# Kernel optimization log

Hardware: AMD Instinct MI355X
Metric: run time of the kernel (lower is better)

## Reference

```python
import jax, jax.numpy as jnp
import numpy as np

B, F, S = 64, 1024, 256
H = 1024  # hidden_size == input_size (required by default forward path)


def setup_inputs() -> dict:
    key = jax.random.key(0)
    k1, k2, k3, k4 = jax.random.split(key, 4)
    stdv = 1.0 / (H ** 0.5)
    x = jax.random.normal(k1, (B, F, S), dtype=jnp.float32)
    W = jax.random.uniform(k2, (F, 4 * H), dtype=jnp.float32, minval=-stdv, maxval=stdv)
    U = jax.random.uniform(k3, (H, 4 * H), dtype=jnp.float32, minval=-stdv, maxval=stdv)
    bias = jax.random.uniform(k4, (4 * H,), dtype=jnp.float32, minval=-stdv, maxval=stdv)
    return {"x": x, "W": W, "U": U, "bias": bias}


def reference(x, W, U, bias):
    # x: [B, F, S]. Faithful to MotionLSTM.forward with init_states=None,
    # isSampling=False, output_frame=0:  c_t = f_t * x_t + i_t * g_t.
    batch, _, seq = x.shape
    HS = U.shape[0]
    # Precompute input projection once: [S, B, 4H]
    xW = jnp.einsum('bfs,fg->sbg', x, W)
    x_seq = jnp.transpose(x, (2, 0, 1))  # [S, B, F]
    h0 = jnp.zeros((batch, HS), dtype=x.dtype)
    c0 = jnp.zeros((batch, HS), dtype=x.dtype)

    def step(carry, inputs):
        h, c = carry
        xw_t, x_t = inputs
        gates = xw_t + h @ U + bias  # [B, 4H]
        i_t = jax.nn.sigmoid(gates[:, :HS])
        f_t = jax.nn.sigmoid(gates[:, HS:2 * HS])
        g_t = jnp.tanh(gates[:, 2 * HS:3 * HS])
        o_t = jax.nn.sigmoid(gates[:, 3 * HS:])
        c_new = f_t * x_t + i_t * g_t  # isSampling=False path
        h_new = o_t * jnp.tanh(c_new)
        return (h_new, c_new), h_new

    (h_T, c_T), hs = jax.lax.scan(step, (h0, c0), (xW, x_seq))
    hidden_seq = jnp.transpose(hs, (1, 2, 0))  # [B, H, S]
    return hidden_seq, h_T, c_T
```

## Files before the change

### kernel.cpp

```cpp
#include <hip/hip_runtime.h>
#include <hip/hip_bf16.h>

typedef float f32x4 __attribute__((ext_vector_type(4)));
typedef short short8 __attribute__((ext_vector_type(8)));
typedef __bf16 bf16x8 __attribute__((ext_vector_type(8)));

#define DI __device__ __forceinline__

constexpr int Bsz = 64;
constexpr int Fd  = 1024;
constexpr int Seq = 256;
constexpr int G4  = 4096;
constexpr int Mrows = Seq * Bsz;

DI float bf2f(unsigned short u) {
  union { unsigned int i; float f; } v; v.i = ((unsigned int)u) << 16; return v.f;
}
DI unsigned short f2bf(float f) {
  union { float ff; unsigned int i; } v; v.ff = f;
  unsigned int x = v.i;
  return (unsigned short)((x + 0x7fffu + ((x >> 16) & 1u)) >> 16);
}
DI float sigm(float x) { return 1.f / (1.f + __expf(-x)); }
DI float tanhfast(float x) {
  float e = __expf(-2.f * fabsf(x));
  float t = (1.f - e) / (1.f + e);
  return x < 0.f ? -t : t;
}
DI f32x4 mfma16(short8 a, short8 b, f32x4 c) {
  return __builtin_amdgcn_mfma_f32_16x16x32_bf16(
      __builtin_bit_cast(bf16x8, a), __builtin_bit_cast(bf16x8, b), c, 0, 0, 0);
}

__global__ void k_tx(const float* __restrict__ x, unsigned short* __restrict__ xs) {
  __shared__ float t[32][33];
  int b = blockIdx.z, f0 = blockIdx.y * 32, s0 = blockIdx.x * 32;
  int tx = threadIdx.x & 31, ty = threadIdx.x >> 5;
  const float* src = x + ((size_t)b * Fd + f0) * Seq + s0;
#pragma unroll
  for (int i = 0; i < 32; i += 8)
    t[ty + i][tx] = src[(size_t)(ty + i) * Seq + tx];
  __syncthreads();
#pragma unroll
  for (int i = 0; i < 32; i += 8) {
    int s = s0 + ty + i, f = f0 + tx;
    xs[((size_t)s * Bsz + b) * Fd + f] = f2bf(t[tx][ty + i]);
  }
}

__global__ void k_tw(const float* __restrict__ in, unsigned short* __restrict__ out) {
  __shared__ float t[32][33];
  int n0 = blockIdx.x * 32, k0 = blockIdx.y * 32;
  int tx = threadIdx.x & 31, ty = threadIdx.x >> 5;
#pragma unroll
  for (int i = 0; i < 32; i += 8)
    t[ty + i][tx] = in[(size_t)(k0 + ty + i) * G4 + n0 + tx];
  __syncthreads();
#pragma unroll
  for (int i = 0; i < 32; i += 8)
    out[(size_t)(n0 + ty + i) * 1024 + k0 + tx] = f2bf(t[tx][ty + i]);
}

__global__ void k_zero(unsigned int* p, int n) {
  int i = blockIdx.x * 256 + threadIdx.x;
  if (i < n) p[i] = 0u;
}

__launch_bounds__(256, 2)
__global__ void k_gemm(const unsigned short* __restrict__ A,
                       const unsigned short* __restrict__ Bt,
                       unsigned short* __restrict__ C) {
  __shared__ unsigned short a_lds[128 * 64];
  __shared__ unsigned short b_lds[128 * 64];
  int bid = blockIdx.x;
  int tm = bid & 127, tn = bid >> 7;
  int tid = threadIdx.x, w = tid >> 6, l = tid & 63;
  int wm = w >> 1, wn = w & 1;
  f32x4 acc[4][4] = {};
  const unsigned short* Ab = A + (size_t)(tm * 128) * 1024;
  const unsigned short* Bb = Bt + (size_t)(tn * 128) * 1024;
  for (int kt = 0; kt < 16; ++kt) {
#pragma unroll
    for (int i = 0; i < 4; ++i) {
      int ci = tid + i * 256;
      int row = ci >> 3;
      int kB = (ci & 7) * 16;
      short8 va = *(const short8*)((const char*)(Ab + (size_t)row * 1024 + kt * 64) + kB);
      short8 vb = *(const short8*)((const char*)(Bb + (size_t)row * 1024 + kt * 64) + kB);
      int dst = row * 128 + (kB ^ ((row & 7) << 4));
      *(short8*)((char*)a_lds + dst) = va;
      *(short8*)((char*)b_lds + dst) = vb;
    }
    __syncthreads();
#pragma unroll
    for (int kb = 0; kb < 2; ++kb) {
      short8 af[4], bfv[4];
      int kByte = (kb * 32 + ((l >> 4) << 3)) * 2;
#pragma unroll
      for (int mi = 0; mi < 4; ++mi) {
        int row = wm * 64 + mi * 16 + (l & 15);
        af[mi] = *(const short8*)((const char*)a_lds + row * 128 + (kByte ^ ((row & 7) << 4)));
      }
#pragma unroll
      for (int ni = 0; ni < 4; ++ni) {
        int row = wn * 64 + ni * 16 + (l & 15);
        bfv[ni] = *(const short8*)((const char*)b_lds + row * 128 + (kByte ^ ((row & 7) << 4)));
      }
#pragma unroll
      for (int mi = 0; mi < 4; ++mi)
#pragma unroll
        for (int ni = 0; ni < 4; ++ni)
          acc[mi][ni] = mfma16(af[mi], bfv[ni], acc[mi][ni]);
    }
    __syncthreads();
  }
#pragma unroll
  for (int mi = 0; mi < 4; ++mi)
#pragma unroll
    for (int ni = 0; ni < 4; ++ni)
#pragma unroll
      for (int r = 0; r < 4; ++r) {
        int m = tm * 128 + wm * 64 + mi * 16 + ((l >> 4) << 2) + r;
        int n = tn * 128 + wn * 64 + ni * 16 + (l & 15);
        C[(size_t)m * G4 + n] = f2bf(acc[mi][ni][r]);
      }
}

__launch_bounds__(256, 1)
__global__ void k_rec(const unsigned short* __restrict__ xs,
                      const unsigned short* __restrict__ xWb,
                      const unsigned short* __restrict__ Ubt,
                      const float* __restrict__ bias,
                      unsigned int* __restrict__ hbuf,
                      unsigned int* tags,
                      float* __restrict__ out) {
  __shared__ unsigned short h_lds[16 * 1024];
  __shared__ float g_lds[16][64];
  __shared__ float obuf[256][17];
  int bid = blockIdx.x;
  int rg = bid & 3, jg = bid >> 2;
  int j0 = jg * 16;
  int tid = threadIdx.x, w = tid >> 6, l = tid & 63;

  int ncol = w * 1024 + j0 + (l & 15);
  const unsigned short* Urow = Ubt + (size_t)ncol * 1024;
  short8 ufr[32];
#pragma unroll
  for (int kb = 0; kb < 32; ++kb)
    ufr[kb] = *(const short8*)(Urow + kb * 32 + ((l >> 4) << 3));
  float bias_l = bias[ncol];

  unsigned int* mytags = tags + rg * 64;
  unsigned int* mytag = mytags + jg;

  int row2 = tid >> 4, jj = tid & 15;
  int bb = rg * 16 + row2, j = j0 + jj;

  for (int t = 0; t < Seq; ++t) {
    float xw[4];
#pragma unroll
    for (int r = 0; r < 4; ++r) {
      int m = rg * 16 + ((l >> 4) << 2) + r;
      xw[r] = bf2f(xWb[((size_t)t * 64 + m) * G4 + ncol]);
    }
    float xt = bf2f(xs[((size_t)t * 64 + bb) * Fd + j]);

    f32x4 acc = {0.f, 0.f, 0.f, 0.f};
    if (t > 0) {
      if (tid < 64) {
        while (__hip_atomic_load(&mytags[tid], __ATOMIC_RELAXED,
                                 __HIP_MEMORY_SCOPE_SYSTEM) < (unsigned int)t) {}
      }
      __syncthreads();
      const unsigned int* hprev = hbuf + (((t & 1) ^ 1) << 15) + (rg << 13);
      unsigned int hv[32];
#pragma unroll
      for (int i = 0; i < 32; ++i)
        hv[i] = __hip_atomic_load(hprev + tid + i * 256, __ATOMIC_RELAXED,
                                  __HIP_MEMORY_SCOPE_SYSTEM);
#pragma unroll
      for (int i = 0; i < 32; ++i) {
        int ci = tid + i * 256;
        int row = ci >> 9, kB = (ci & 511) * 4;
        *(unsigned int*)((char*)h_lds + row * 2048 + (kB ^ ((row & 7) << 4))) = hv[i];
      }
      __syncthreads();
#pragma unroll
      for (int kb = 0; kb < 32; ++kb) {
        int row = l & 15;
        int kByte = (kb * 32 + ((l >> 4) << 3)) * 2;
        short8 af = *(const short8*)((const char*)h_lds + row * 2048 +
                                     (kByte ^ ((row & 7) << 4)));
        acc = mfma16(af, ufr[kb], acc);
      }
    }
#pragma unroll
    for (int r = 0; r < 4; ++r)
      g_lds[((l >> 4) << 2) + r][w * 16 + (l & 15)] = acc[r] + xw[r] + bias_l;
    __syncthreads();
    float iv = g_lds[row2][jj];
    float fv = g_lds[row2][16 + jj];
    float gv = g_lds[row2][32 + jj];
    float ov = g_lds[row2][48 + jj];
    float si = sigm(iv), sf = sigm(fv), tg = tanhfast(gv), so = sigm(ov);
    float c = sf * xt + si * tg;
    float h = so * tanhfast(c);
    unsigned short hb = f2bf(h);
    unsigned int other = (unsigned int)(unsigned short)__shfl_xor((int)(unsigned int)hb, 1);
    if ((jj & 1) == 0) {
      unsigned int u = (unsigned int)hb | (other << 16);
      __hip_atomic_store(hbuf + ((t & 1) << 15) + (bb << 9) + (j >> 1), u,
                         __ATOMIC_RELAXED, __HIP_MEMORY_SCOPE_SYSTEM);
    }
    obuf[tid][t & 15] = h;
    if (t == Seq - 1) {
      out[(size_t)16777216 + (size_t)bb * 1024 + j] = h;
      out[(size_t)16777216 + 65536 + (size_t)bb * 1024 + j] = c;
    }
    asm volatile("s_waitcnt vmcnt(0)" ::: "memory");
    __syncthreads();
    if (tid == 0)
      __hip_atomic_store(mytag, (unsigned int)(t + 1), __ATOMIC_RELAXED,
                         __HIP_MEMORY_SCOPE_SYSTEM);
    if ((t & 15) == 15) {
      float* dst = out + ((size_t)bb * 1024 + j) * Seq + (t - 15);
#pragma unroll
      for (int q = 0; q < 4; ++q) {
        f32x4 v = {obuf[tid][q * 4], obuf[tid][q * 4 + 1],
                   obuf[tid][q * 4 + 2], obuf[tid][q * 4 + 3]};
        *(f32x4*)(dst + q * 4) = v;
      }
    }
  }
}

extern "C" void kernel_launch(void* const* d_in, const int* in_sizes, int n_in,
                              void* d_out, int out_size, void* d_ws, size_t ws_size,
                              hipStream_t stream) {
  const float* x    = (const float*)d_in[0];
  const float* W    = (const float*)d_in[1];
  const float* U    = (const float*)d_in[2];
  const float* bias = (const float*)d_in[3];
  float* out = (float*)d_out;
  char* ws = (char*)d_ws;

  unsigned short* xs  = (unsigned short*)(ws);
  unsigned short* Wbt = (unsigned short*)(ws + (size_t)33554432);
  unsigned short* Ubt = (unsigned short*)(ws + (size_t)41943040);
  unsigned short* xWb = (unsigned short*)(ws + (size_t)50331648);
  unsigned int* hbuf  = (unsigned int*)(ws + (size_t)184549376);
  unsigned int* tags  = (unsigned int*)(ws + (size_t)184811520);

  k_tx<<<dim3(Seq / 32, Fd / 32, Bsz), 256, 0, stream>>>(x, xs);
  k_tw<<<dim3(G4 / 32, 1024 / 32), 256, 0, stream>>>(W, Wbt);
  k_tw<<<dim3(G4 / 32, 1024 / 32), 256, 0, stream>>>(U, Ubt);
  k_zero<<<1, 256, 0, stream>>>(tags, 256);
  k_gemm<<<dim3((Mrows / 128) * (G4 / 128)), 256, 0, stream>>>(xs, Wbt, xWb);
  k_rec<<<dim3(256), 256, 0, stream>>>(xs, xWb, Ubt, bias, hbuf, tags, out);
}
```

Before: 969.7 us.

## Halve recurrence blocks to 128 with 512 threads and vectorized h loads

The persistent recurrent kernel now uses 128 blocks of 512 threads instead of 256 blocks of 256. Each block owns 32 hidden columns, which halves the number of producers each block must poll per step and halves redundant loads of h into shared memory. The h gather now uses four 16-byte system-coherent loads per thread through inline assembly, and the MFMA chain is split into two accumulators to shorten the dependency chain. In exchange, each block holds more U registers, the output flush happens every 8 steps, and per-CU occupancy and register pressure change.

```diff
diff --git a/kernel.cpp b/kernel.cpp
--- a/kernel.cpp
+++ b/kernel.cpp
@@ -4,6 +4,7 @@
 typedef float f32x4 __attribute__((ext_vector_type(4)));
 typedef short short8 __attribute__((ext_vector_type(8)));
 typedef __bf16 bf16x8 __attribute__((ext_vector_type(8)));
+typedef unsigned int u32x4 __attribute__((ext_vector_type(4)));
 
 #define DI __device__ __forceinline__
 
@@ -30,6 +31,20 @@
 DI f32x4 mfma16(short8 a, short8 b, f32x4 c) {
   return __builtin_amdgcn_mfma_f32_16x16x32_bf16(
       __builtin_bit_cast(bf16x8, a), __builtin_bit_cast(bf16x8, b), c, 0, 0, 0);
+}
+
+DI void ld4x4_sys(const unsigned int* p0, const unsigned int* p1,
+                  const unsigned int* p2, const unsigned int* p3,
+                  u32x4& a, u32x4& b, u32x4& c, u32x4& d) {
+  asm volatile(
+      "global_load_dwordx4 %0, %4, off sc0 sc1\n\t"
+      "global_load_dwordx4 %1, %5, off sc0 sc1\n\t"
+      "global_load_dwordx4 %2, %6, off sc0 sc1\n\t"
+      "global_load_dwordx4 %3, %7, off sc0 sc1\n\t"
+      "s_waitcnt vmcnt(0)"
+      : "=&v"(a), "=&v"(b), "=&v"(c), "=&v"(d)
+      : "v"(p0), "v"(p1), "v"(p2), "v"(p3)
+      : "memory");
 }
 
 __global__ void k_tx(const float* __restrict__ x, unsigned short* __restrict__ xs) {
@@ -126,23 +141,25 @@
       }
 }
 
-__launch_bounds__(256, 1)
+__launch_bounds__(512, 2)
 __global__ void k_rec(const unsigned short* __restrict__ xs,
                       const unsigned short* __restrict__ xWb,
                       const unsigned short* __restrict__ Ubt,
                       const float* __restrict__ bias,
                       unsigned int* __restrict__ hbuf,
-                      unsigned int* tags,
+                      unsigned int* __restrict__ tags,
                       float* __restrict__ out) {
   __shared__ unsigned short h_lds[16 * 1024];
-  __shared__ float g_lds[16][64];
-  __shared__ float obuf[256][17];
+  __shared__ float g_lds[16][132];
+  __shared__ float obuf[512][9];
   int bid = blockIdx.x;
-  int rg = bid & 3, jg = bid >> 2;
-  int j0 = jg * 16;
+  int rg = bid & 3, ch = bid >> 2;
   int tid = threadIdx.x, w = tid >> 6, l = tid & 63;
-
-  int ncol = w * 1024 + j0 + (l & 15);
+  int g = w >> 1, cs = w & 1;
+  int jloc = cs * 16 + (l & 15);
+  int ncol = g * 1024 + ch * 32 + jloc;
+  int mrow0 = (l >> 4) << 2;
+
   const unsigned short* Urow = Ubt + (size_t)ncol * 1024;
   short8 ufr[32];
 #pragma unroll
@@ -150,82 +167,86 @@
     ufr[kb] = *(const short8*)(Urow + kb * 32 + ((l >> 4) << 3));
   float bias_l = bias[ncol];
 
-  unsigned int* mytags = tags + rg * 64;
-  unsigned int* mytag = mytags + jg;
-
-  int row2 = tid >> 4, jj = tid & 15;
-  int bb = rg * 16 + row2, j = j0 + jj;
+  unsigned int* mytags = tags + rg * 32;
+  unsigned int* mytag = mytags + ch;
+
+  int prow = tid >> 5, pj = tid & 31;
+  int pb = rg * 16 + prow;
+  int pjglob = ch * 32 + pj;
 
   for (int t = 0; t < Seq; ++t) {
     float xw[4];
 #pragma unroll
-    for (int r = 0; r < 4; ++r) {
-      int m = rg * 16 + ((l >> 4) << 2) + r;
-      xw[r] = bf2f(xWb[((size_t)t * 64 + m) * G4 + ncol]);
-    }
-    float xt = bf2f(xs[((size_t)t * 64 + bb) * Fd + j]);
-
-    f32x4 acc = {0.f, 0.f, 0.f, 0.f};
+    for (int r = 0; r < 4; ++r)
+      xw[r] = bf2f(xWb[((size_t)t * 64 + rg * 16 + mrow0 + r) * G4 + ncol]);
+    float xt = bf2f(xs[((size_t)t * 64 + pb) * Fd + pjglob]);
+
+    f32x4 acc0 = {0.f, 0.f, 0.f, 0.f}, acc1 = {0.f, 0.f, 0.f, 0.f};
     if (t > 0) {
-      if (tid < 64) {
+      if (tid < 32) {
         while (__hip_atomic_load(&mytags[tid], __ATOMIC_RELAXED,
                                  __HIP_MEMORY_SCOPE_SYSTEM) < (unsigned int)t) {}
       }
       __syncthreads();
-      const unsigned int* hprev = hbuf + (((t & 1) ^ 1) << 15) + (rg << 13);
-      unsigned int hv[32];
-#pragma unroll
-      for (int i = 0; i < 32; ++i)
-        hv[i] = __hip_atomic_load(hprev + tid + i * 256, __ATOMIC_RELAXED,
-                                  __HIP_MEMORY_SCOPE_SYSTEM);
-#pragma unroll
-      for (int i = 0; i < 32; ++i) {
-        int ci = tid + i * 256;
-        int row = ci >> 9, kB = (ci & 511) * 4;
-        *(unsigned int*)((char*)h_lds + row * 2048 + (kB ^ ((row & 7) << 4))) = hv[i];
+      const unsigned int* hp = hbuf + (((t & 1) ^ 1) << 15) + (rg << 13);
+      u32x4 h0, h1, h2, h3;
+      ld4x4_sys(hp + tid * 4, hp + 2048 + tid * 4, hp + 4096 + tid * 4,
+                hp + 6144 + tid * 4, h0, h1, h2, h3);
+      __builtin_amdgcn_sched_barrier(0);
+      {
+        int c0 = tid;        int r0 = c0 >> 7, b0 = (c0 & 127) * 16;
+        *(u32x4*)((char*)h_lds + r0 * 2048 + (b0 ^ ((r0 & 7) << 4))) = h0;
+        int c1 = tid + 512;  int r1 = c1 >> 7, b1 = (c1 & 127) * 16;
+        *(u32x4*)((char*)h_lds + r1 * 2048 + (b1 ^ ((r1 & 7) << 4))) = h1;
+        int c2 = tid + 1024; int r2 = c2 >> 7, b2 = (c2 & 127) * 16;
+        *(u32x4*)((char*)h_lds + r2 * 2048 + (b2 ^ ((r2 & 7) << 4))) = h2;
+        int c3 = tid + 1536; int r3 = c3 >> 7, b3 = (c3 & 127) * 16;
+        *(u32x4*)((char*)h_lds + r3 * 2048 + (b3 ^ ((r3 & 7) << 4))) = h3;
       }
       __syncthreads();
-#pragma unroll
-      for (int kb = 0; kb < 32; ++kb) {
-        int row = l & 15;
-        int kByte = (kb * 32 + ((l >> 4) << 3)) * 2;
-        short8 af = *(const short8*)((const char*)h_lds + row * 2048 +
-                                     (kByte ^ ((row & 7) << 4)));
-        acc = mfma16(af, ufr[kb], acc);
+      int arow = l & 15;
+      const char* abase = (const char*)h_lds + arow * 2048;
+      int sw = (arow & 7) << 4;
+      int kres = (l >> 4) << 4;
+#pragma unroll
+      for (int kb = 0; kb < 32; kb += 2) {
+        short8 a0 = *(const short8*)(abase + ((kb * 64 + kres) ^ sw));
+        acc0 = mfma16(a0, ufr[kb], acc0);
+        short8 a1 = *(const short8*)(abase + (((kb + 1) * 64 + kres) ^ sw));
+        acc1 = mfma16(a1, ufr[kb + 1], acc1);
       }
     }
 #pragma unroll
     for (int r = 0; r < 4; ++r)
-      g_lds[((l >> 4) << 2) + r][w * 16 + (l & 15)] = acc[r] + xw[r] + bias_l;
-    __syncthreads();
-    float iv = g_lds[row2][jj];
-    float fv = g_lds[row2][16 + jj];
-    float gv = g_lds[row2][32 + jj];
-    float ov = g_lds[row2][48 + jj];
+      g_lds[mrow0 + r][g * 32 + jloc] = acc0[r] + acc1[r] + xw[r] + bias_l;
+    __syncthreads();
+    float iv = g_lds[prow][pj];
+    float fv = g_lds[prow][32 + pj];
+    float gv = g_lds[prow][64 + pj];
+    float ov = g_lds[prow][96 + pj];
     float si = sigm(iv), sf = sigm(fv), tg = tanhfast(gv), so = sigm(ov);
-    float c = sf * xt + si * tg;
-    float h = so * tanhfast(c);
-    unsigned short hb = f2bf(h);
-    unsigned int other = (unsigned int)(unsigned short)__shfl_xor((int)(unsigned int)hb, 1);
-    if ((jj & 1) == 0) {
-      unsigned int u = (unsigned int)hb | (other << 16);
-      __hip_atomic_store(hbuf + ((t & 1) << 15) + (bb << 9) + (j >> 1), u,
-                         __ATOMIC_RELAXED, __HIP_MEMORY_SCOPE_SYSTEM);
-    }
-    obuf[tid][t & 15] = h;
+    float cval = sf * xt + si * tg;
+    float hval = so * tanhfast(cval);
+    obuf[tid][t & 7] = hval;
+    unsigned int me = f2bf(hval);
+    unsigned int ot = (unsigned int)__shfl_xor((int)me, 1) & 0xffffu;
+    if ((pj & 1) == 0)
+      __hip_atomic_store(hbuf + ((t & 1) << 15) + pb * 512 + (pjglob >> 1),
+                         me | (ot << 16), __ATOMIC_RELAXED,
+                         __HIP_MEMORY_SCOPE_SYSTEM);
     if (t == Seq - 1) {
-      out[(size_t)16777216 + (size_t)bb * 1024 + j] = h;
-      out[(size_t)16777216 + 65536 + (size_t)bb * 1024 + j] = c;
+      out[(size_t)16777216 + (size_t)pb * 1024 + pjglob] = hval;
+      out[(size_t)16777216 + 65536 + (size_t)pb * 1024 + pjglob] = cval;
     }
     asm volatile("s_waitcnt vmcnt(0)" ::: "memory");
     __syncthreads();
     if (tid == 0)
       __hip_atomic_store(mytag, (unsigned int)(t + 1), __ATOMIC_RELAXED,
                          __HIP_MEMORY_SCOPE_SYSTEM);
-    if ((t & 15) == 15) {
-      float* dst = out + ((size_t)bb * 1024 + j) * Seq + (t - 15);
-#pragma unroll
-      for (int q = 0; q < 4; ++q) {
+    if ((t & 7) == 7) {
+      float* dst = out + ((size_t)pb * 1024 + pjglob) * Seq + (t - 7);
+#pragma unroll
+      for (int q = 0; q < 2; ++q) {
         f32x4 v = {obuf[tid][q * 4], obuf[tid][q * 4 + 1],
                    obuf[tid][q * 4 + 2], obuf[tid][q * 4 + 3]};
         *(f32x4*)(dst + q * 4) = v;
@@ -256,5 +277,5 @@
   k_tw<<<dim3(G4 / 32, 1024 / 32), 256, 0, stream>>>(U, Ubt);
   k_zero<<<1, 256, 0, stream>>>(tags, 256);
   k_gemm<<<dim3((Mrows / 128) * (G4 / 128)), 256, 0, stream>>>(xs, Wbt, xWb);
-  k_rec<<<dim3(256), 256, 0, stream>>>(xs, xWb, Ubt, bias, hbuf, tags, out);
-}
+  k_rec<<<dim3(128), 512, 0, stream>>>(xs, xWb, Ubt, bias, hbuf, tags, out);
+}
```

Measured after the change: 1.026 ms. 1.06x slower.

## Use a tagged 32-slot ring for h exchange with validated plain loads

Applied to the files above, without the earlier changes.

The hidden-state exchange buffer becomes a 32-slot ring in the workspace, reusing the bf16 W region once the GEMM is done. Each h element is stored as its own dword carrying a step tag, written with sc0 sc1 stores. Readers use plain vector loads and check the tags, falling back to sc0 sc1 reloads when stale data is seen. The MFMA reduction is split into two accumulators, and optional diagnostic variants (no-sync and comm-only modes) launch only when the workspace is large enough. The aim is to cut the cost of system-scope atomic loads per step, at the price of twice the exchange traffic and the extra tag checks.

```diff
diff --git a/kernel.cpp b/kernel.cpp
--- a/kernel.cpp
+++ b/kernel.cpp
@@ -4,6 +4,8 @@
 typedef float f32x4 __attribute__((ext_vector_type(4)));
 typedef short short8 __attribute__((ext_vector_type(8)));
 typedef __bf16 bf16x8 __attribute__((ext_vector_type(8)));
+typedef unsigned int u32x4 __attribute__((ext_vector_type(4)));
+typedef unsigned int u32x2 __attribute__((ext_vector_type(2)));
 
 #define DI __device__ __forceinline__
 
@@ -36,10 +38,9 @@
   __shared__ float t[32][33];
   int b = blockIdx.z, f0 = blockIdx.y * 32, s0 = blockIdx.x * 32;
   int tx = threadIdx.x & 31, ty = threadIdx.x >> 5;
-  const float* src = x + ((size_t)b * Fd + f0) * Seq + s0;
 #pragma unroll
   for (int i = 0; i < 32; i += 8)
-    t[ty + i][tx] = src[(size_t)(ty + i) * Seq + tx];
+    t[ty + i][tx] = x[((size_t)b * Fd + f0 + ty + i) * Seq + s0 + tx];
   __syncthreads();
 #pragma unroll
   for (int i = 0; i < 32; i += 8) {
@@ -126,14 +127,16 @@
       }
 }
 
+template <int MODE>
 __launch_bounds__(256, 1)
 __global__ void k_rec(const unsigned short* __restrict__ xs,
                       const unsigned short* __restrict__ xWb,
                       const unsigned short* __restrict__ Ubt,
                       const float* __restrict__ bias,
-                      unsigned int* __restrict__ hbuf,
-                      unsigned int* tags,
-                      float* __restrict__ out) {
+                      unsigned int* __restrict__ ring,
+                      unsigned int* __restrict__ tags,
+                      float* __restrict__ out,
+                      int nsteps) {
   __shared__ unsigned short h_lds[16 * 1024];
   __shared__ float g_lds[16][64];
   __shared__ float obuf[256][17];
@@ -154,76 +157,114 @@
   unsigned int* mytag = mytags + jg;
 
   int row2 = tid >> 4, jj = tid & 15;
-  int bb = rg * 16 + row2, j = j0 + jj;
-
-  for (int t = 0; t < Seq; ++t) {
+  int pb = rg * 16 + row2, pj = j0 + jj;
+
+  for (int t = 0; t < nsteps; ++t) {
     float xw[4];
 #pragma unroll
     for (int r = 0; r < 4; ++r) {
       int m = rg * 16 + ((l >> 4) << 2) + r;
       xw[r] = bf2f(xWb[((size_t)t * 64 + m) * G4 + ncol]);
     }
-    float xt = bf2f(xs[((size_t)t * 64 + bb) * Fd + j]);
-
-    f32x4 acc = {0.f, 0.f, 0.f, 0.f};
+    float xt = bf2f(xs[((size_t)t * 64 + pb) * Fd + pj]);
+
+    f32x4 acc0 = {0.f, 0.f, 0.f, 0.f}, acc1 = {0.f, 0.f, 0.f, 0.f};
     if (t > 0) {
-      if (tid < 64) {
-        while (__hip_atomic_load(&mytags[tid], __ATOMIC_RELAXED,
-                                 __HIP_MEMORY_SCOPE_SYSTEM) < (unsigned int)t) {}
-      }
+      if (MODE != 1) {
+        if (tid < 64) {
+          while (__hip_atomic_load(&mytags[tid], __ATOMIC_RELAXED,
+                                   __HIP_MEMORY_SCOPE_SYSTEM) < (unsigned int)t) {}
+        }
+        __syncthreads();
+        __builtin_amdgcn_sched_barrier(0);
+      }
+      const unsigned int* hb_t = ring + (((t - 1) & 31) << 16) + (rg << 14);
+      unsigned int expect = (MODE == 2) ? ((unsigned int)t | 0x8000u) : (unsigned int)t;
+      int slow = 0;
+      for (;;) {
+        u32x4 hv[16];
+        if (!slow) {
+#pragma unroll
+          for (int k = 0; k < 16; ++k)
+            hv[k] = *(const u32x4*)(hb_t + k * 1024 + tid * 4);
+        } else {
+#pragma unroll
+          for (int k = 0; k < 16; ++k)
+            asm volatile("global_load_dwordx4 %0, %1, off sc0 sc1"
+                         : "=v"(hv[k]) : "v"(hb_t + k * 1024 + tid * 4));
+          asm volatile("s_waitcnt vmcnt(0)" ::: "memory");
+        }
+        unsigned int bad = 0u;
+        if (MODE != 1) {
+#pragma unroll
+          for (int k = 0; k < 16; ++k)
+#pragma unroll
+            for (int q = 0; q < 4; ++q)
+              bad |= (hv[k][q] >> 16) ^ expect;
+        }
+#pragma unroll
+        for (int k = 0; k < 16; ++k) {
+          u32x2 pk;
+          pk[0] = (hv[k][0] & 0xffffu) | (hv[k][1] << 16);
+          pk[1] = (hv[k][2] & 0xffffu) | (hv[k][3] << 16);
+          *(u32x2*)((char*)h_lds + k * 2048 + ((tid * 8) ^ ((k & 7) << 4))) = pk;
+        }
+        if (__syncthreads_and((int)(bad == 0u))) break;
+        slow = 1;
+      }
+      if (MODE != 2) {
+        int arow = l & 15;
+        const char* abase = (const char*)h_lds + arow * 2048;
+        int sw = (arow & 7) << 4;
+        int kres = (l >> 4) << 4;
+#pragma unroll
+        for (int kb = 0; kb < 32; kb += 2) {
+          short8 a0 = *(const short8*)(abase + ((kb * 64 + kres) ^ sw));
+          acc0 = mfma16(a0, ufr[kb], acc0);
+          short8 a1 = *(const short8*)(abase + (((kb + 1) * 64 + kres) ^ sw));
+          acc1 = mfma16(a1, ufr[kb + 1], acc1);
+        }
+      }
+    }
+    if (MODE != 2) {
+#pragma unroll
+      for (int r = 0; r < 4; ++r)
+        g_lds[((l >> 4) << 2) + r][w * 16 + (l & 15)] = acc0[r] + acc1[r] + xw[r] + bias_l;
       __syncthreads();
-      const unsigned int* hprev = hbuf + (((t & 1) ^ 1) << 15) + (rg << 13);
-      unsigned int hv[32];
-#pragma unroll
-      for (int i = 0; i < 32; ++i)
-        hv[i] = __hip_atomic_load(hprev + tid + i * 256, __ATOMIC_RELAXED,
-                                  __HIP_MEMORY_SCOPE_SYSTEM);
-#pragma unroll
-      for (int i = 0; i < 32; ++i) {
-        int ci = tid + i * 256;
-        int row = ci >> 9, kB = (ci & 511) * 4;
-        *(unsigned int*)((char*)h_lds + row * 2048 + (kB ^ ((row & 7) << 4))) = hv[i];
-      }
+      float iv = g_lds[row2][jj];
+      float fv = g_lds[row2][16 + jj];
+      float gv = g_lds[row2][32 + jj];
+      float ov = g_lds[row2][48 + jj];
+      float si = sigm(iv), sf = sigm(fv), tg = tanhfast(gv), so = sigm(ov);
+      float cval = sf * xt + si * tg;
+      float hval = so * tanhfast(cval);
+      obuf[tid][t & 15] = hval;
+      unsigned int tagged = (unsigned int)f2bf(hval) | ((unsigned int)(t + 1) << 16);
+      unsigned int* hp = ring + ((t & 31) << 16) + (pb << 10) + pj;
+      asm volatile("global_store_dword %0, %1, off sc0 sc1"
+                   :: "v"(hp), "v"(tagged) : "memory");
+      if (MODE == 0 && t == nsteps - 1) {
+        out[(size_t)16777216 + (size_t)pb * 1024 + pj] = hval;
+        out[(size_t)16777216 + 65536 + (size_t)pb * 1024 + pj] = cval;
+      }
+      if (MODE == 1 && t == nsteps - 1)
+        out[((size_t)pb * 1024 + pj) & 0x3ffc0] = hval + cval;
+    } else {
+      unsigned int tagged = ((unsigned int)(t + 1) | 0x8000u) << 16;
+      unsigned int* hp = ring + ((t & 31) << 16) + (pb << 10) + pj;
+      asm volatile("global_store_dword %0, %1, off sc0 sc1"
+                   :: "v"(hp), "v"(tagged) : "memory");
+    }
+    if (MODE != 1) {
+      asm volatile("s_waitcnt vmcnt(0)" ::: "memory");
       __syncthreads();
-#pragma unroll
-      for (int kb = 0; kb < 32; ++kb) {
-        int row = l & 15;
-        int kByte = (kb * 32 + ((l >> 4) << 3)) * 2;
-        short8 af = *(const short8*)((const char*)h_lds + row * 2048 +
-                                     (kByte ^ ((row & 7) << 4)));
-        acc = mfma16(af, ufr[kb], acc);
-      }
-    }
-#pragma unroll
-    for (int r = 0; r < 4; ++r)
-      g_lds[((l >> 4) << 2) + r][w * 16 + (l & 15)] = acc[r] + xw[r] + bias_l;
-    __syncthreads();
-    float iv = g_lds[row2][jj];
-    float fv = g_lds[row2][16 + jj];
-    float gv = g_lds[row2][32 + jj];
-    float ov = g_lds[row2][48 + jj];
-    float si = sigm(iv), sf = sigm(fv), tg = tanhfast(gv), so = sigm(ov);
-    float c = sf * xt + si * tg;
-    float h = so * tanhfast(c);
-    unsigned short hb = f2bf(h);
-    unsigned int other = (unsigned int)(unsigned short)__shfl_xor((int)(unsigned int)hb, 1);
-    if ((jj & 1) == 0) {
-      unsigned int u = (unsigned int)hb | (other << 16);
-      __hip_atomic_store(hbuf + ((t & 1) << 15) + (bb << 9) + (j >> 1), u,
-                         __ATOMIC_RELAXED, __HIP_MEMORY_SCOPE_SYSTEM);
-    }
-    obuf[tid][t & 15] = h;
-    if (t == Seq - 1) {
-      out[(size_t)16777216 + (size_t)bb * 1024 + j] = h;
-      out[(size_t)16777216 + 65536 + (size_t)bb * 1024 + j] = c;
-    }
-    asm volatile("s_waitcnt vmcnt(0)" ::: "memory");
-    __syncthreads();
-    if (tid == 0)
-      __hip_atomic_store(mytag, (unsigned int)(t + 1), __ATOMIC_RELAXED,
-                         __HIP_MEMORY_SCOPE_SYSTEM);
-    if ((t & 15) == 15) {
-      float* dst = out + ((size_t)bb * 1024 + j) * Seq + (t - 15);
+      if (tid == 0)
+        __hip_atomic_store(mytag, (unsigned int)(t + 1), __ATOMIC_RELAXED,
+                           __HIP_MEMORY_SCOPE_SYSTEM);
+    }
+    if (MODE != 2 && (t & 15) == 15) {
+      size_t idx = ((size_t)pb * 1024 + pj) * Seq + (t - 15);
+      float* dst = (MODE == 0) ? (out + idx) : (out + (idx & 0x3ffc0));
 #pragma unroll
       for (int q = 0; q < 4; ++q) {
         f32x4 v = {obuf[tid][q * 4], obuf[tid][q * 4 + 1],
@@ -248,13 +289,27 @@
   unsigned short* Wbt = (unsigned short*)(ws + (size_t)33554432);
   unsigned short* Ubt = (unsigned short*)(ws + (size_t)41943040);
   unsigned short* xWb = (unsigned short*)(ws + (size_t)50331648);
-  unsigned int* hbuf  = (unsigned int*)(ws + (size_t)184549376);
-  unsigned int* tags  = (unsigned int*)(ws + (size_t)184811520);
+  unsigned int* ring  = (unsigned int*)(ws + (size_t)33554432);
+  unsigned int* tags  = (unsigned int*)(ws + (size_t)184549376);
+
+  bool diag = ws_size >= (size_t)212 * 1024 * 1024;
+  unsigned int* hbuf2 = (unsigned int*)(ws + (size_t)192 * 1024 * 1024);
+  unsigned int* hbuf3 = (unsigned int*)(ws + (size_t)200 * 1024 * 1024);
+  unsigned int* tags2 = (unsigned int*)(ws + (size_t)208 * 1024 * 1024);
+  float* diag_out     = (float*)(ws + (size_t)209 * 1024 * 1024);
 
   k_tx<<<dim3(Seq / 32, Fd / 32, Bsz), 256, 0, stream>>>(x, xs);
   k_tw<<<dim3(G4 / 32, 1024 / 32), 256, 0, stream>>>(W, Wbt);
   k_tw<<<dim3(G4 / 32, 1024 / 32), 256, 0, stream>>>(U, Ubt);
   k_zero<<<1, 256, 0, stream>>>(tags, 256);
+  if (diag) {
+    k_zero<<<1, 256, 0, stream>>>(tags2, 256);
+    k_zero<<<8192, 256, 0, stream>>>(hbuf3, 1 << 21);
+  }
   k_gemm<<<dim3((Mrows / 128) * (G4 / 128)), 256, 0, stream>>>(xs, Wbt, xWb);
-  k_rec<<<dim3(256), 256, 0, stream>>>(xs, xWb, Ubt, bias, hbuf, tags, out);
-}
+  k_rec<0><<<dim3(256), 256, 0, stream>>>(xs, xWb, Ubt, bias, ring, tags, out, Seq);
+  if (diag) {
+    k_rec<1><<<dim3(256), 256, 0, stream>>>(xs, xWb, Ubt, bias, hbuf2, tags2, diag_out, 64);
+    k_rec<2><<<dim3(256), 256, 0, stream>>>(xs, xWb, Ubt, bias, hbuf3, tags2, diag_out, 64);
+  }
+}
```

New measurement: 1.622 ms. 67.3% more time.

## Embed step-parity check bits in h values and load h with vector loads

Applied to the files above, without the earlier changes.

Each stored bf16 h value now has its two low mantissa bits replaced by a step-dependent pattern. Readers load h with wide dwordx4 cache-bypassing loads and retry any chunk whose check bits do not yet match the expected step. This removes the s_waitcnt before the tag store and replaces 32 scalar atomic loads with 8 vector loads. The MFMA chain is split into four independent accumulators and the gate LDS array is padded. The cost is two bits of h precision, plus a correctness dependency on the tag/check protocol, since the tag is now stored without waiting for the h stores to complete.

```diff
diff --git a/kernel.cpp b/kernel.cpp
--- a/kernel.cpp
+++ b/kernel.cpp
@@ -4,6 +4,7 @@
 typedef float f32x4 __attribute__((ext_vector_type(4)));
 typedef short short8 __attribute__((ext_vector_type(8)));
 typedef __bf16 bf16x8 __attribute__((ext_vector_type(8)));
+typedef unsigned int u32x4 __attribute__((ext_vector_type(4)));
 
 #define DI __device__ __forceinline__
 
@@ -36,10 +37,9 @@
   __shared__ float t[32][33];
   int b = blockIdx.z, f0 = blockIdx.y * 32, s0 = blockIdx.x * 32;
   int tx = threadIdx.x & 31, ty = threadIdx.x >> 5;
-  const float* src = x + ((size_t)b * Fd + f0) * Seq + s0;
 #pragma unroll
   for (int i = 0; i < 32; i += 8)
-    t[ty + i][tx] = src[(size_t)(ty + i) * Seq + tx];
+    t[ty + i][tx] = x[((size_t)b * Fd + f0 + ty + i) * Seq + s0 + tx];
   __syncthreads();
 #pragma unroll
   for (int i = 0; i < 32; i += 8) {
@@ -132,10 +132,10 @@
                       const unsigned short* __restrict__ Ubt,
                       const float* __restrict__ bias,
                       unsigned int* __restrict__ hbuf,
-                      unsigned int* tags,
+                      unsigned int* __restrict__ tags,
                       float* __restrict__ out) {
   __shared__ unsigned short h_lds[16 * 1024];
-  __shared__ float g_lds[16][64];
+  __shared__ float g_lds[16][68];
   __shared__ float obuf[256][17];
   int bid = blockIdx.x;
   int rg = bid & 3, jg = bid >> 2;
@@ -154,7 +154,16 @@
   unsigned int* mytag = mytags + jg;
 
   int row2 = tid >> 4, jj = tid & 15;
-  int bb = rg * 16 + row2, j = j0 + jj;
+  int pb = rg * 16 + row2, pj = j0 + jj;
+
+  int fsrc[8], fdst[8];
+#pragma unroll
+  for (int i = 0; i < 8; ++i) {
+    int ci = tid + i * 256;
+    int row = ci >> 7;
+    fsrc[i] = row * 512 + (ci & 127) * 4;
+    fdst[i] = row * 2048 + (((ci & 127) * 16) ^ ((row & 7) << 4));
+  }
 
   for (int t = 0; t < Seq; ++t) {
     float xw[4];
@@ -163,67 +172,99 @@
       int m = rg * 16 + ((l >> 4) << 2) + r;
       xw[r] = bf2f(xWb[((size_t)t * 64 + m) * G4 + ncol]);
     }
-    float xt = bf2f(xs[((size_t)t * 64 + bb) * Fd + j]);
-
-    f32x4 acc = {0.f, 0.f, 0.f, 0.f};
+    float xt = bf2f(xs[((size_t)t * 64 + pb) * Fd + pj]);
+
+    f32x4 acc0 = {0.f, 0.f, 0.f, 0.f}, acc1 = {0.f, 0.f, 0.f, 0.f};
+    f32x4 acc2 = {0.f, 0.f, 0.f, 0.f}, acc3 = {0.f, 0.f, 0.f, 0.f};
     if (t > 0) {
       if (tid < 64) {
         while (__hip_atomic_load(&mytags[tid], __ATOMIC_RELAXED,
                                  __HIP_MEMORY_SCOPE_SYSTEM) < (unsigned int)t) {}
       }
       __syncthreads();
-      const unsigned int* hprev = hbuf + (((t & 1) ^ 1) << 15) + (rg << 13);
-      unsigned int hv[32];
-#pragma unroll
-      for (int i = 0; i < 32; ++i)
-        hv[i] = __hip_atomic_load(hprev + tid + i * 256, __ATOMIC_RELAXED,
-                                  __HIP_MEMORY_SCOPE_SYSTEM);
-#pragma unroll
-      for (int i = 0; i < 32; ++i) {
-        int ci = tid + i * 256;
-        int row = ci >> 9, kB = (ci & 511) * 4;
-        *(unsigned int*)((char*)h_lds + row * 2048 + (kB ^ ((row & 7) << 4))) = hv[i];
-      }
+      __builtin_amdgcn_sched_barrier(0);
+      const unsigned int* hb_base = hbuf + (((t & 1) ^ 1) << 15) + (rg << 13);
+      u32x4 cv[8];
+#pragma unroll
+      for (int i = 0; i < 8; ++i)
+        asm volatile("global_load_dwordx4 %0, %1, off sc0 sc1"
+                     : "=v"(cv[i]) : "v"(hb_base + fsrc[i]));
+      asm volatile("s_waitcnt vmcnt(0)" ::: "memory");
+      unsigned int tm1 = (unsigned int)(t - 1);
+      unsigned int pat = (tm1 & 3u) | ((3u - (tm1 & 3u)) << 16);
+      for (;;) {
+        unsigned int badm = 0u;
+#pragma unroll
+        for (int i = 0; i < 8; ++i) {
+          unsigned int bm = 0u;
+#pragma unroll
+          for (int q = 0; q < 4; ++q)
+            bm |= (cv[i][q] & 0x00030003u) ^ pat;
+          badm |= (bm ? 1u : 0u) << i;
+        }
+        if (!__any(badm != 0u)) break;
+#pragma unroll
+        for (int i = 0; i < 8; ++i)
+          if (badm & (1u << i))
+            asm volatile("global_load_dwordx4 %0, %1, off sc0 sc1"
+                         : "=v"(cv[i]) : "v"(hb_base + fsrc[i]));
+        asm volatile("s_waitcnt vmcnt(0)" ::: "memory");
+      }
+#pragma unroll
+      for (int i = 0; i < 8; ++i)
+        *(u32x4*)((char*)h_lds + fdst[i]) = cv[i];
       __syncthreads();
-#pragma unroll
-      for (int kb = 0; kb < 32; ++kb) {
-        int row = l & 15;
-        int kByte = (kb * 32 + ((l >> 4) << 3)) * 2;
-        short8 af = *(const short8*)((const char*)h_lds + row * 2048 +
-                                     (kByte ^ ((row & 7) << 4)));
-        acc = mfma16(af, ufr[kb], acc);
+      int arow = l & 15;
+      const char* abase = (const char*)h_lds + arow * 2048;
+      int sw = (arow & 7) << 4;
+      int kres = (l >> 4) << 4;
+#pragma unroll
+      for (int kb = 0; kb < 32; kb += 4) {
+        short8 a0 = *(const short8*)(abase + ((kb * 64 + kres) ^ sw));
+        acc0 = mfma16(a0, ufr[kb], acc0);
+        short8 a1 = *(const short8*)(abase + (((kb + 1) * 64 + kres) ^ sw));
+        acc1 = mfma16(a1, ufr[kb + 1], acc1);
+        short8 a2 = *(const short8*)(abase + (((kb + 2) * 64 + kres) ^ sw));
+        acc2 = mfma16(a2, ufr[kb + 2], acc2);
+        short8 a3 = *(const short8*)(abase + (((kb + 3) * 64 + kres) ^ sw));
+        acc3 = mfma16(a3, ufr[kb + 3], acc3);
       }
     }
 #pragma unroll
     for (int r = 0; r < 4; ++r)
-      g_lds[((l >> 4) << 2) + r][w * 16 + (l & 15)] = acc[r] + xw[r] + bias_l;
+      g_lds[((l >> 4) << 2) + r][w * 16 + (l & 15)] =
+          acc0[r] + acc1[r] + acc2[r] + acc3[r] + xw[r] + bias_l;
     __syncthreads();
     float iv = g_lds[row2][jj];
     float fv = g_lds[row2][16 + jj];
     float gv = g_lds[row2][32 + jj];
     float ov = g_lds[row2][48 + jj];
     float si = sigm(iv), sf = sigm(fv), tg = tanhfast(gv), so = sigm(ov);
-    float c = sf * xt + si * tg;
-    float h = so * tanhfast(c);
-    unsigned short hb = f2bf(h);
-    unsigned int other = (unsigned int)(unsigned short)__shfl_xor((int)(unsigned int)hb, 1);
-    if ((jj & 1) == 0) {
-      unsigned int u = (unsigned int)hb | (other << 16);
-      __hip_atomic_store(hbuf + ((t & 1) << 15) + (bb << 9) + (j >> 1), u,
-                         __ATOMIC_RELAXED, __HIP_MEMORY_SCOPE_SYSTEM);
-    }
-    obuf[tid][t & 15] = h;
+    float cval = sf * xt + si * tg;
+    float hval = so * tanhfast(cval);
+    obuf[tid][t & 15] = hval;
+    {
+      unsigned int chk = (jj & 1) ? (3u - ((unsigned int)t & 3u))
+                                  : ((unsigned int)t & 3u);
+      unsigned int hb = ((unsigned int)f2bf(hval) & 0xFFFCu) | chk;
+      unsigned int ot = (unsigned int)__shfl_xor((int)hb, 1) & 0xFFFFu;
+      if ((jj & 1) == 0) {
+        unsigned int u = hb | (ot << 16);
+        unsigned int* hp = hbuf + ((t & 1) << 15) + (pb << 9) + (pj >> 1);
+        asm volatile("global_store_dword %0, %1, off sc0 sc1"
+                     :: "v"(hp), "v"(u) : "memory");
+      }
+    }
     if (t == Seq - 1) {
-      out[(size_t)16777216 + (size_t)bb * 1024 + j] = h;
-      out[(size_t)16777216 + 65536 + (size_t)bb * 1024 + j] = c;
-    }
-    asm volatile("s_waitcnt vmcnt(0)" ::: "memory");
+      out[(size_t)16777216 + (size_t)pb * 1024 + pj] = hval;
+      out[(size_t)16777216 + 65536 + (size_t)pb * 1024 + pj] = cval;
+    }
     __syncthreads();
     if (tid == 0)
       __hip_atomic_store(mytag, (unsigned int)(t + 1), __ATOMIC_RELAXED,
                          __HIP_MEMORY_SCOPE_SYSTEM);
     if ((t & 15) == 15) {
-      float* dst = out + ((size_t)bb * 1024 + j) * Seq + (t - 15);
+      float* dst = out + ((size_t)pb * 1024 + pj) * Seq + (t - 15);
 #pragma unroll
       for (int q = 0; q < 4; ++q) {
         f32x4 v = {obuf[tid][q * 4], obuf[tid][q * 4 + 1],
```

New measurement: 1.009 ms. +4.1%, slower.
